# Optimization experiments

Measured on AMD Instinct MI355X. Metric: run time of the kernel, lower is better.

## Reference

```python
import jax, jax.numpy as jnp
import numpy as np

T, N = 64, 2048          # timesteps, population
DT = 1e-3                # simulation step
TAU_MEM_INV = 100.0      # LIF membrane 1/tau
V_TH, V_LEAK, V_RESET = 1.0, 0.0, 0.0
TAU_PRE_INV, TAU_POST_INV = 50.0, 50.0   # STDP trace 1/tau
A_PRE, A_POST = 1.0, 1.0                 # trace contributions
ETA_PLUS, ETA_MINUS = 1e-3, 1e-3         # learning rates
W_MIN, W_MAX = 0.0, 1.0                  # hard bounds
ALPHA = 100.0                            # SuperSpike surrogate sharpness

@jax.custom_vjp
def spike(v):
    # Heaviside forward, SuperSpike surrogate backward (as in norse LIF cells)
    return (v > 0.0).astype(v.dtype)

def _spike_fwd(v):
    return spike(v), v

def _spike_bwd(v, g):
    return (g / (ALPHA * jnp.abs(v) + 1.0) ** 2,)

spike.defvjp(_spike_fwd, _spike_bwd)


def setup_inputs() -> dict:
    key = jax.random.key(0)
    k1, k2 = jax.random.split(key)
    # +1.0 bias ensures nonzero spiking activity so STDP actually fires
    exc_current = jax.random.normal(k1, (T, N), dtype=jnp.float32) + 1.0
    # recurrent weights w[post, pre], small positive init within [W_MIN, W_MAX]
    w = jax.random.uniform(k2, (N, N), dtype=jnp.float32) * 0.02
    t_pre = jnp.zeros((N,), jnp.float32)
    t_post = jnp.zeros((N,), jnp.float32)
    return {"exc_current": exc_current, "w": w, "t_pre": t_pre, "t_post": t_post}


def reference(exc_current, w, t_pre, t_post):
    n = w.shape[0]
    z0 = jnp.zeros((n,), w.dtype)  # Layer reset: cell(zeros(population))
    v0 = jnp.zeros((n,), w.dtype)

    def step(carry, x):
        w_, z, v, tp, tpo = carry
        # recurrent synaptic current: w[post, pre] @ z_pre
        i_syn = w_ @ z
        # LIF membrane update
        v = v + DT * TAU_MEM_INV * ((V_LEAK - v) + i_syn + x)
        z_new = spike(v - V_TH)
        v = v * (1.0 - z_new) + V_RESET * z_new  # reset
        # STDP traces (norse stdp_step_linear: update traces, then dw)
        tp = tp + DT * TAU_PRE_INV * (-tp + A_PRE * z_new)
        tpo = tpo + DT * TAU_POST_INV * (-tpo + A_POST * z_new)
        dw = ETA_PLUS * jnp.outer(z_new, tp) - ETA_MINUS * jnp.outer(tpo, z_new)
        w_ = jnp.clip(w_ + dw, W_MIN, W_MAX)  # additive STDP, hard bounds
        return (w_, z_new, v, tp, tpo), z_new

    _, spikes = jax.lax.scan(step, (w, z0, v0, t_pre, t_post), exc_current)
    return spikes  # [T, N], matches torch.stack([self.step(x) for x in exc_current])
```

## Files before the change

kernel.cpp:

```cpp
#include <hip/hip_runtime.h>

constexpr int   T_STEPS = 64;
constexpr int   NN      = 2048;
constexpr float DT_TAU  = 0.1f;
constexpr float V_TH_C  = 1.0f;
constexpr float TRC     = 0.05f;
constexpr float ETA     = 1e-3f;

constexpr int BLOCKS  = 256;
constexpr int THREADS = 512;
constexpr int ROWS_PER_BLOCK = NN / BLOCKS;
constexpr int CHUNKS = NN / 256;

__global__ __launch_bounds__(THREADS)
void snn_msg_kernel(const float* __restrict__ x,
                    const float* __restrict__ w_in,
                    const float* __restrict__ tpre0,
                    const float* __restrict__ tpost0,
                    unsigned long long* __restrict__ zpub,
                    float*       __restrict__ out)
{
    const int bid  = blockIdx.x;
    const int tid  = threadIdx.x;
    const int wv   = tid >> 6;
    const int lane = tid & 63;
    const int row  = bid * ROWS_PER_BLOCK + wv;

    __shared__ __align__(16) float z_s[NN];
    __shared__ __align__(16) float tp_s[NN];
    __shared__ float tpo_s8[ROWS_PER_BLOCK];
    __shared__ float isyn_s8[ROWS_PER_BLOCK];
    __shared__ unsigned zw_s[BLOCKS];

    float4 tp4 = ((const float4*)tpre0)[tid];
    ((float4*)tp_s)[tid] = tp4;

    float v_own = 0.0f, tpo_own = 0.0f, x_own = 0.0f;
    if (tid < ROWS_PER_BLOCK) {
        tpo_own = tpost0[bid * ROWS_PER_BLOCK + tid];
        isyn_s8[tid] = 0.0f;
        x_own = x[bid * ROWS_PER_BLOCK + tid];
    }

    const float4* wrow4 = (const float4*)(w_in + (size_t)row * NN);
    float4 wreg[CHUNKS];
    #pragma unroll
    for (int c = 0; c < CHUNKS; ++c) wreg[c] = wrow4[c * 64 + lane];

    __syncthreads();

    for (int t = 0; t < T_STEPS; ++t) {
        const int par = t & 1;

        if (tid < 64) {
            float z = 0.0f;
            if (tid < ROWS_PER_BLOCK) {
                float v = v_own;
                v = v + DT_TAU * ((0.0f - v) + isyn_s8[tid] + x_own);
                z = (v - V_TH_C > 0.0f) ? 1.0f : 0.0f;
                v_own = v * (1.0f - z);
                tpo_own = tpo_own + TRC * (-tpo_own + z);
                tpo_s8[tid] = tpo_own;
            }
            unsigned long long bits = __ballot(z > 0.0f) & 0xFFull;
            if (tid == 0) {
                unsigned long long word =
                    ((unsigned long long)(unsigned)t << 32) | bits;
                __hip_atomic_store(&zpub[par * BLOCKS + bid], word,
                                   __ATOMIC_RELAXED, __HIP_MEMORY_SCOPE_AGENT);
            }
            if (tid < ROWS_PER_BLOCK) {
                int tn = (t + 1 < T_STEPS) ? t + 1 : t;
                x_own = x[(size_t)tn * NN + bid * ROWS_PER_BLOCK + tid];
            }
        }

        if (tid < BLOCKS) {
            unsigned long long v;
            do {
                v = __hip_atomic_load(&zpub[par * BLOCKS + tid],
                                      __ATOMIC_RELAXED, __HIP_MEMORY_SCOPE_AGENT);
            } while ((unsigned)(v >> 32) != (unsigned)t);
            zw_s[tid] = (unsigned)v;
        }
        __syncthreads();

        {
            unsigned wbits = zw_s[tid >> 1];
            int sh = (tid & 1) * 4;
            float4 z4;
            z4.x = ((wbits >> (sh + 0)) & 1u) ? 1.0f : 0.0f;
            z4.y = ((wbits >> (sh + 1)) & 1u) ? 1.0f : 0.0f;
            z4.z = ((wbits >> (sh + 2)) & 1u) ? 1.0f : 0.0f;
            z4.w = ((wbits >> (sh + 3)) & 1u) ? 1.0f : 0.0f;
            ((float4*)z_s)[tid] = z4;
            tp4.x = tp4.x + TRC * (-tp4.x + z4.x);
            tp4.y = tp4.y + TRC * (-tp4.y + z4.y);
            tp4.z = tp4.z + TRC * (-tp4.z + z4.z);
            tp4.w = tp4.w + TRC * (-tp4.w + z4.w);
            ((float4*)tp_s)[tid] = tp4;
            if (bid == 0) ((float4*)(out + (size_t)t * NN))[tid] = z4;
        }
        __syncthreads();

        if (t == T_STEPS - 1) break;

        const float zi   = z_s[row];
        const float tpoi = tpo_s8[wv];
        float acc = 0.0f;
        const float4* z4s  = (const float4*)z_s;
        const float4* tp4s = (const float4*)tp_s;
        #pragma unroll
        for (int c = 0; c < CHUNKS; ++c) {
            float4 zj = z4s[c * 64 + lane];
            float4 tj = tp4s[c * 64 + lane];
            float nw;
            nw = wreg[c].x + (ETA * (zi * tj.x) - ETA * (tpoi * zj.x));
            nw = fminf(fmaxf(nw, 0.0f), 1.0f); wreg[c].x = nw; acc += nw * zj.x;
            nw = wreg[c].y + (ETA * (zi * tj.y) - ETA * (tpoi * zj.y));
            nw = fminf(fmaxf(nw, 0.0f), 1.0f); wreg[c].y = nw; acc += nw * zj.y;
            nw = wreg[c].z + (ETA * (zi * tj.z) - ETA * (tpoi * zj.z));
            nw = fminf(fmaxf(nw, 0.0f), 1.0f); wreg[c].z = nw; acc += nw * zj.z;
            nw = wreg[c].w + (ETA * (zi * tj.w) - ETA * (tpoi * zj.w));
            nw = fminf(fmaxf(nw, 0.0f), 1.0f); wreg[c].w = nw; acc += nw * zj.w;
        }
        #pragma unroll
        for (int m = 32; m >= 1; m >>= 1) acc += __shfl_xor(acc, m, 64);
        if (lane == 0) isyn_s8[wv] = acc;
        __syncthreads();
    }
}

extern "C" void kernel_launch(void* const* d_in, const int* in_sizes, int n_in,
                              void* d_out, int out_size, void* d_ws, size_t ws_size,
                              hipStream_t stream) {
    const float* x     = (const float*)d_in[0];
    const float* w_in  = (const float*)d_in[1];
    const float* tpre  = (const float*)d_in[2];
    const float* tpost = (const float*)d_in[3];
    float*       out   = (float*)d_out;

    unsigned long long* zpub = (unsigned long long*)d_ws;

    void* args[] = {(void*)&x, (void*)&w_in, (void*)&tpre, (void*)&tpost,
                    (void*)&zpub, (void*)&out};
    hipLaunchCooperativeKernel((void*)snn_msg_kernel,
                               dim3(BLOCKS), dim3(THREADS),
                               args, 0, stream);
}
```

Measured before the change: 325.5 us.

## Compact spike flags to 32-bit words and poll them with vector loads in one wave

The per-block spike publication word shrinks from 64-bit to 32-bit, packing the step tag into the upper bits. A single wavefront now polls all 256 flags with dwordx4 loads that bypass the cache (sc0 sc1), instead of 256 threads each spinning on their own 64-bit atomic load. The input current for all timesteps is preloaded into shared memory, removing the per-step global load. Each block writes its own output spikes, and the last step skips the publish and wait entirely. The inline assembly polling depends on GFX9-style cache control bits, and the 24-bit step tag assumes the workspace starts cleared or holds stale tags that never match.

```diff
diff --git a/kernel.cpp b/kernel.cpp
--- a/kernel.cpp
+++ b/kernel.cpp
@@ -12,12 +12,14 @@
 constexpr int ROWS_PER_BLOCK = NN / BLOCKS;
 constexpr int CHUNKS = NN / 256;
 
+typedef unsigned int uint4v __attribute__((ext_vector_type(4)));
+
 __global__ __launch_bounds__(THREADS)
 void snn_msg_kernel(const float* __restrict__ x,
                     const float* __restrict__ w_in,
                     const float* __restrict__ tpre0,
                     const float* __restrict__ tpost0,
-                    unsigned long long* __restrict__ zpub,
+                    unsigned*    __restrict__ zpub,
                     float*       __restrict__ out)
 {
     const int bid  = blockIdx.x;
@@ -28,18 +30,20 @@
 
     __shared__ __align__(16) float z_s[NN];
     __shared__ __align__(16) float tp_s[NN];
+    __shared__ __align__(16) float x_s[T_STEPS * ROWS_PER_BLOCK];
+    __shared__ __align__(16) unsigned zw_s[BLOCKS];
     __shared__ float tpo_s8[ROWS_PER_BLOCK];
     __shared__ float isyn_s8[ROWS_PER_BLOCK];
-    __shared__ unsigned zw_s[BLOCKS];
 
     float4 tp4 = ((const float4*)tpre0)[tid];
     ((float4*)tp_s)[tid] = tp4;
 
-    float v_own = 0.0f, tpo_own = 0.0f, x_own = 0.0f;
+    x_s[tid] = x[(size_t)(tid >> 3) * NN + bid * ROWS_PER_BLOCK + (tid & 7)];
+
+    float v_own = 0.0f, tpo_own = 0.0f;
     if (tid < ROWS_PER_BLOCK) {
         tpo_own = tpost0[bid * ROWS_PER_BLOCK + tid];
         isyn_s8[tid] = 0.0f;
-        x_own = x[bid * ROWS_PER_BLOCK + tid];
     }
 
     const float4* wrow4 = (const float4*)(w_in + (size_t)row * NN);
@@ -56,32 +60,38 @@
             float z = 0.0f;
             if (tid < ROWS_PER_BLOCK) {
                 float v = v_own;
-                v = v + DT_TAU * ((0.0f - v) + isyn_s8[tid] + x_own);
+                v = v + DT_TAU * ((0.0f - v) + isyn_s8[tid]
+                                  + x_s[t * ROWS_PER_BLOCK + tid]);
                 z = (v - V_TH_C > 0.0f) ? 1.0f : 0.0f;
                 v_own = v * (1.0f - z);
                 tpo_own = tpo_own + TRC * (-tpo_own + z);
                 tpo_s8[tid] = tpo_own;
+                out[(size_t)t * NN + bid * ROWS_PER_BLOCK + tid] = z;
             }
-            unsigned long long bits = __ballot(z > 0.0f) & 0xFFull;
-            if (tid == 0) {
-                unsigned long long word =
-                    ((unsigned long long)(unsigned)t << 32) | bits;
-                __hip_atomic_store(&zpub[par * BLOCKS + bid], word,
-                                   __ATOMIC_RELAXED, __HIP_MEMORY_SCOPE_AGENT);
-            }
-            if (tid < ROWS_PER_BLOCK) {
-                int tn = (t + 1 < T_STEPS) ? t + 1 : t;
-                x_own = x[(size_t)tn * NN + bid * ROWS_PER_BLOCK + tid];
+            if (t + 1 < T_STEPS) {
+                unsigned long long bits = __ballot(z > 0.0f) & 0xFFull;
+                if (tid == 0) {
+                    unsigned word = ((unsigned)(t + 1) << 8) | (unsigned)bits;
+                    __hip_atomic_store(&zpub[par * BLOCKS + bid], word,
+                                       __ATOMIC_RELAXED, __HIP_MEMORY_SCOPE_AGENT);
+                }
             }
         }
+        if (t == T_STEPS - 1) break;
 
-        if (tid < BLOCKS) {
-            unsigned long long v;
+        if (wv == 1) {
+            const unsigned expect = (unsigned)(t + 1);
+            const unsigned* p = zpub + par * BLOCKS + 4 * lane;
+            uint4v w;
+            bool done = false;
             do {
-                v = __hip_atomic_load(&zpub[par * BLOCKS + tid],
-                                      __ATOMIC_RELAXED, __HIP_MEMORY_SCOPE_AGENT);
-            } while ((unsigned)(v >> 32) != (unsigned)t);
-            zw_s[tid] = (unsigned)v;
+                asm volatile("global_load_dwordx4 %0, %1, off sc0 sc1\n\t"
+                             "s_waitcnt vmcnt(0)"
+                             : "=v"(w) : "v"(p) : "memory");
+                done = ((w.x >> 8) == expect) & ((w.y >> 8) == expect) &
+                       ((w.z >> 8) == expect) & ((w.w >> 8) == expect);
+            } while (!done);
+            *(uint4v*)&zw_s[4 * lane] = w;
         }
         __syncthreads();
 
@@ -99,11 +109,8 @@
             tp4.z = tp4.z + TRC * (-tp4.z + z4.z);
             tp4.w = tp4.w + TRC * (-tp4.w + z4.w);
             ((float4*)tp_s)[tid] = tp4;
-            if (bid == 0) ((float4*)(out + (size_t)t * NN))[tid] = z4;
         }
         __syncthreads();
-
-        if (t == T_STEPS - 1) break;
 
         const float zi   = z_s[row];
         const float tpoi = tpo_s8[wv];
@@ -140,7 +147,7 @@
     const float* tpost = (const float*)d_in[3];
     float*       out   = (float*)d_out;
 
-    unsigned long long* zpub = (unsigned long long*)d_ws;
+    unsigned* zpub = (unsigned*)d_ws;
 
     void* args[] = {(void*)&x, (void*)&w_in, (void*)&tpre, (void*)&tpost,
                     (void*)&zpub, (void*)&out};
```

New measurement: 366.1 us. 12.5% more time.

## Pad spike mailboxes, preload inputs to LDS, and add backoff to the exchange spin

Applied to the files above, without the earlier changes.

Spike-publish slots are spaced by a stride (up to 16 words) chosen from the workspace size, so each block's mailbox sits on its own cache line and polling avoids false sharing. All per-block input currents are loaded into shared memory once at start, removing the global load on the critical path each step. Each block writes its own spike outputs directly instead of block 0 writing the whole row, and the final step skips the exchange. Pollers add s_sleep backoff, which cuts memory traffic but can add wake-up latency to the per-step barrier.

```diff
diff --git a/kernel.cpp b/kernel.cpp
--- a/kernel.cpp
+++ b/kernel.cpp
@@ -18,6 +18,7 @@
                     const float* __restrict__ tpre0,
                     const float* __restrict__ tpost0,
                     unsigned long long* __restrict__ zpub,
+                    int stride,
                     float*       __restrict__ out)
 {
     const int bid  = blockIdx.x;
@@ -28,18 +29,20 @@
 
     __shared__ __align__(16) float z_s[NN];
     __shared__ __align__(16) float tp_s[NN];
+    __shared__ __align__(16) float x_s[T_STEPS * ROWS_PER_BLOCK];
+    __shared__ unsigned zw_s[BLOCKS];
     __shared__ float tpo_s8[ROWS_PER_BLOCK];
     __shared__ float isyn_s8[ROWS_PER_BLOCK];
-    __shared__ unsigned zw_s[BLOCKS];
 
     float4 tp4 = ((const float4*)tpre0)[tid];
     ((float4*)tp_s)[tid] = tp4;
 
-    float v_own = 0.0f, tpo_own = 0.0f, x_own = 0.0f;
+    x_s[tid] = x[(size_t)(tid >> 3) * NN + bid * ROWS_PER_BLOCK + (tid & 7)];
+
+    float v_own = 0.0f, tpo_own = 0.0f;
     if (tid < ROWS_PER_BLOCK) {
         tpo_own = tpost0[bid * ROWS_PER_BLOCK + tid];
         isyn_s8[tid] = 0.0f;
-        x_own = x[bid * ROWS_PER_BLOCK + tid];
     }
 
     const float4* wrow4 = (const float4*)(w_in + (size_t)row * NN);
@@ -54,33 +57,40 @@
 
         if (tid < 64) {
             float z = 0.0f;
+            float v = 0.0f;
             if (tid < ROWS_PER_BLOCK) {
-                float v = v_own;
-                v = v + DT_TAU * ((0.0f - v) + isyn_s8[tid] + x_own);
+                v = v_own;
+                v = v + DT_TAU * ((0.0f - v) + isyn_s8[tid]
+                                  + x_s[t * ROWS_PER_BLOCK + tid]);
                 z = (v - V_TH_C > 0.0f) ? 1.0f : 0.0f;
-                v_own = v * (1.0f - z);
+            }
+            unsigned long long bits = __ballot(z > 0.0f) & 0xFFull;
+            if (t + 1 < T_STEPS && tid == 0) {
+                unsigned long long word =
+                    ((unsigned long long)(unsigned)(t + 1) << 32) | bits;
+                __hip_atomic_store(&zpub[(size_t)(par * BLOCKS + bid) * stride],
+                                   word, __ATOMIC_RELAXED,
+                                   __HIP_MEMORY_SCOPE_AGENT);
+            }
+            if (tid < ROWS_PER_BLOCK) {
+                v_own   = v * (1.0f - z);
                 tpo_own = tpo_own + TRC * (-tpo_own + z);
                 tpo_s8[tid] = tpo_own;
-            }
-            unsigned long long bits = __ballot(z > 0.0f) & 0xFFull;
-            if (tid == 0) {
-                unsigned long long word =
-                    ((unsigned long long)(unsigned)t << 32) | bits;
-                __hip_atomic_store(&zpub[par * BLOCKS + bid], word,
-                                   __ATOMIC_RELAXED, __HIP_MEMORY_SCOPE_AGENT);
-            }
-            if (tid < ROWS_PER_BLOCK) {
-                int tn = (t + 1 < T_STEPS) ? t + 1 : t;
-                x_own = x[(size_t)tn * NN + bid * ROWS_PER_BLOCK + tid];
+                out[(size_t)t * NN + bid * ROWS_PER_BLOCK + tid] = z;
             }
         }
+        if (t == T_STEPS - 1) break;
 
         if (tid < BLOCKS) {
-            unsigned long long v;
-            do {
-                v = __hip_atomic_load(&zpub[par * BLOCKS + tid],
-                                      __ATOMIC_RELAXED, __HIP_MEMORY_SCOPE_AGENT);
-            } while ((unsigned)(v >> 32) != (unsigned)t);
+            const unsigned long long* p =
+                &zpub[(size_t)(par * BLOCKS + tid) * stride];
+            unsigned long long v =
+                __hip_atomic_load(p, __ATOMIC_RELAXED, __HIP_MEMORY_SCOPE_AGENT);
+            while ((unsigned)(v >> 32) != (unsigned)(t + 1)) {
+                asm volatile("s_sleep 1");
+                v = __hip_atomic_load(p, __ATOMIC_RELAXED,
+                                      __HIP_MEMORY_SCOPE_AGENT);
+            }
             zw_s[tid] = (unsigned)v;
         }
         __syncthreads();
@@ -99,11 +109,8 @@
             tp4.z = tp4.z + TRC * (-tp4.z + z4.z);
             tp4.w = tp4.w + TRC * (-tp4.w + z4.w);
             ((float4*)tp_s)[tid] = tp4;
-            if (bid == 0) ((float4*)(out + (size_t)t * NN))[tid] = z4;
         }
         __syncthreads();
-
-        if (t == T_STEPS - 1) break;
 
         const float zi   = z_s[row];
         const float tpoi = tpo_s8[wv];
@@ -142,8 +149,13 @@
 
     unsigned long long* zpub = (unsigned long long*)d_ws;
 
+    int stride;
+    if      (ws_size >= (size_t)2 * BLOCKS * 16 * sizeof(unsigned long long)) stride = 16;
+    else if (ws_size >= (size_t)2 * BLOCKS *  8 * sizeof(unsigned long long)) stride = 8;
+    else                                                                      stride = 1;
+
     void* args[] = {(void*)&x, (void*)&w_in, (void*)&tpre, (void*)&tpost,
-                    (void*)&zpub, (void*)&out};
+                    (void*)&zpub, (void*)&stride, (void*)&out};
     hipLaunchCooperativeKernel((void*)snn_msg_kernel,
                                dim3(BLOCKS), dim3(THREADS),
                                args, 0, stream);
```

Measured after the change: 282.3 us. 13.3% less time.
